# Optimization experiments

Measured on AMD Instinct MI355X. Metric: run time of the kernel, lower is better.

## Reference

```python
import jax, jax.numpy as jnp
import numpy as np

N_NODES = 50000
N_EDGES = 800000
N_GRAPHS = 2000
F = 256          # node feature dim == hidden_dim (required by stacked convs)
HID = 256
L = 4
FP = 1034
BN_EPS = 1e-5


def setup_inputs() -> dict:
    key = jax.random.key(0)
    ks = jax.random.split(key, 20)
    s = 0.05
    x = jax.random.normal(ks[0], (N_NODES, F), dtype=jnp.float32)
    edge_index = jax.random.randint(ks[1], (2, N_EDGES), 0, N_NODES, dtype=jnp.int64)
    edge_attr = jax.random.normal(ks[2], (N_EDGES, 1), dtype=jnp.float32)
    fingerprint = jax.random.uniform(ks[3], (N_GRAPHS, FP), dtype=jnp.float32)
    batch = jnp.sort(jax.random.randint(ks[4], (N_NODES,), 0, N_GRAPHS, dtype=jnp.int64))
    # stacked per-layer conv params: message linear [(F+1)->HID], update linear [HID->HID]
    lin_w = jax.random.normal(ks[5], (L, F + 1, HID), dtype=jnp.float32) * s
    lin_b = jax.random.normal(ks[6], (L, HID), dtype=jnp.float32) * s
    upd_w = jax.random.normal(ks[7], (L, HID, HID), dtype=jnp.float32) * s
    upd_b = jax.random.normal(ks[8], (L, HID), dtype=jnp.float32) * s
    # gated-attention pooling gate_nn: Linear(HID,HID) -> tanh -> Linear(HID,1)
    g1_w = jax.random.normal(ks[9], (HID, HID), dtype=jnp.float32) * s
    g1_b = jax.random.normal(ks[10], (HID,), dtype=jnp.float32) * s
    g2_w = jax.random.normal(ks[11], (HID, 1), dtype=jnp.float32) * s
    g2_b = jax.random.normal(ks[12], (1,), dtype=jnp.float32) * s
    fc1_w = jax.random.normal(ks[13], (HID + FP, HID), dtype=jnp.float32) * s
    fc1_b = jax.random.normal(ks[14], (HID,), dtype=jnp.float32) * s
    bn_gamma = jnp.ones((HID,), dtype=jnp.float32)
    bn_beta = jnp.zeros((HID,), dtype=jnp.float32)
    fc2_w = jax.random.normal(ks[15], (HID, 1), dtype=jnp.float32) * s
    fc2_b = jax.random.normal(ks[16], (1,), dtype=jnp.float32) * s
    return dict(x=x, edge_index=edge_index, edge_attr=edge_attr,
                fingerprint=fingerprint, batch=batch,
                lin_w=lin_w, lin_b=lin_b, upd_w=upd_w, upd_b=upd_b,
                g1_w=g1_w, g1_b=g1_b, g2_w=g2_w, g2_b=g2_b,
                fc1_w=fc1_w, fc1_b=fc1_b, bn_gamma=bn_gamma, bn_beta=bn_beta,
                fc2_w=fc2_w, fc2_b=fc2_b)


def reference(x, edge_index, edge_attr, fingerprint, batch,
              lin_w, lin_b, upd_w, upd_b,
              g1_w, g1_b, g2_w, g2_b,
              fc1_w, fc1_b, bn_gamma, bn_beta, fc2_w, fc2_b):
    n = x.shape[0]
    b = fingerprint.shape[0]
    loop = jnp.arange(n, dtype=edge_index.dtype)
    src = jnp.concatenate([edge_index[0], loop])   # x_j = source nodes (PyG default)
    dst = jnp.concatenate([edge_index[1], loop])   # aggregate at target
    ea = jnp.concatenate([edge_attr, jnp.zeros((n, edge_attr.shape[1]), edge_attr.dtype)], axis=0)
    for l in range(L):
        wn, we = lin_w[l, :F], lin_w[l, F:]        # split concat([x_j, edge_attr]) @ W
        msg = jax.nn.relu(x[src] @ wn + ea @ we + lin_b[l])          # [E+n, HID]
        aggr = jax.ops.segment_sum(msg, dst, num_segments=n)          # scatter-add
        x = jax.nn.relu(aggr @ upd_w[l] + upd_b[l])
    # gated attention pooling
    gate = jax.nn.sigmoid(jnp.tanh(x @ g1_w + g1_b) @ g2_w + g2_b)    # [n, 1]
    pooled = jax.ops.segment_sum(x * gate, batch, num_segments=b)     # [b, HID]
    h = jnp.concatenate([pooled, fingerprint], axis=1) @ fc1_w + fc1_b
    # BatchNorm1d (training mode: biased batch stats)
    mu = jnp.mean(h, axis=0)
    var = jnp.mean((h - mu) ** 2, axis=0)
    h = (h - mu) * jax.lax.rsqrt(var + BN_EPS) * bn_gamma + bn_beta
    h = jax.nn.relu(h)  # dropout is identity in eval mode
    return (h @ fc2_w + fc2_b).squeeze(-1)        # [b]
```

## Files before the change

### kernel.cpp

```cpp
#include <hip/hip_runtime.h>
#include <math.h>

#define HIDF 256
#define FPDIM 1034
#define MPAD 50048

typedef _Float16 f16x8 __attribute__((ext_vector_type(8)));
typedef _Float16 f16x4 __attribute__((ext_vector_type(4)));
typedef float f32x4 __attribute__((ext_vector_type(4)));

__device__ __forceinline__ float relu_f(float v) { return fmaxf(v, 0.f); }

__global__ __launch_bounds__(256) void convxh_k(
    const float* __restrict__ x, _Float16* __restrict__ xh, int n)
{
    int i = blockIdx.x * 256 + threadIdx.x;
    int row = i >> 6;
    if (row >= MPAD) return;
    f16x4 o;
    if (row < n) {
        float4 v = ((const float4*)x)[i];
        o[0] = (_Float16)v.x; o[1] = (_Float16)v.y;
        o[2] = (_Float16)v.z; o[3] = (_Float16)v.w;
    } else {
        o[0] = o[1] = o[2] = o[3] = (_Float16)0.f;
    }
    ((f16x4*)xh)[i] = o;
}

__global__ __launch_bounds__(256) void convw_k(
    const float* __restrict__ w, _Float16* __restrict__ whi,
    _Float16* __restrict__ wlo)
{
    int i = blockIdx.x * 256 + threadIdx.x;
    int nn = i >> 8, kk = i & 255;
    float v = w[kk * 256 + nn];
    _Float16 h = (_Float16)v;
    _Float16 l = (_Float16)(v - (float)h);
    whi[i] = h;
    wlo[i] = l;
}

template <int ACT>
__global__ __launch_bounds__(256) void gemm_f16(
    const _Float16* __restrict__ A, const _Float16* __restrict__ Whi,
    const _Float16* __restrict__ Wlo, const float* __restrict__ bias,
    _Float16* __restrict__ C, int M, int N, int K)
{
    __shared__ _Float16 As[128 * 64];
    __shared__ _Float16 Bh[128 * 64];
    __shared__ _Float16 Bl[128 * 64];
    const int tid = threadIdx.x;
    const int wave = tid >> 6, lane = tid & 63;
    const int m0 = blockIdx.y * 128, n0 = blockIdx.x * 128;
    const int wr = wave >> 1, wc = wave & 1;

    f32x4 acc[4][4];
#pragma unroll
    for (int i = 0; i < 4; ++i)
#pragma unroll
        for (int j = 0; j < 4; ++j) acc[i][j] = (f32x4){0.f, 0.f, 0.f, 0.f};

    const int lrow = lane >> 3;
    const int lcol8 = (lane & 7) * 8;

    for (int k0 = 0; k0 < K; k0 += 64) {
#pragma unroll
        for (int i = 0; i < 4; ++i) {
            int iss = wave * 4 + i;
            int row = 8 * iss + lrow;
            const _Float16* ga = A   + (size_t)(m0 + row) * K + k0 + lcol8;
            const _Float16* gh = Whi + (size_t)(n0 + row) * K + k0 + lcol8;
            const _Float16* gl = Wlo + (size_t)(n0 + row) * K + k0 + lcol8;
            __builtin_amdgcn_global_load_lds(
                (const __attribute__((address_space(1))) void*)ga,
                (__attribute__((address_space(3))) void*)(As + iss * 512), 16, 0, 0);
            __builtin_amdgcn_global_load_lds(
                (const __attribute__((address_space(1))) void*)gh,
                (__attribute__((address_space(3))) void*)(Bh + iss * 512), 16, 0, 0);
            __builtin_amdgcn_global_load_lds(
                (const __attribute__((address_space(1))) void*)gl,
                (__attribute__((address_space(3))) void*)(Bl + iss * 512), 16, 0, 0);
        }
        __syncthreads();
#pragma unroll
        for (int kk = 0; kk < 2; ++kk) {
            const int kb = kk * 32 + (lane >> 4) * 8;
            f16x8 af[4], bh[4], bl[4];
#pragma unroll
            for (int mi = 0; mi < 4; ++mi)
                af[mi] = *(const f16x8*)&As[(wr * 64 + mi * 16 + (lane & 15)) * 64 + kb];
#pragma unroll
            for (int ni = 0; ni < 4; ++ni) {
                int r = (wc * 64 + ni * 16 + (lane & 15)) * 64 + kb;
                bh[ni] = *(const f16x8*)&Bh[r];
                bl[ni] = *(const f16x8*)&Bl[r];
            }
#pragma unroll
            for (int mi = 0; mi < 4; ++mi)
#pragma unroll
                for (int ni = 0; ni < 4; ++ni) {
                    acc[mi][ni] = __builtin_amdgcn_mfma_f32_16x16x32_f16(
                        af[mi], bh[ni], acc[mi][ni], 0, 0, 0);
                    acc[mi][ni] = __builtin_amdgcn_mfma_f32_16x16x32_f16(
                        af[mi], bl[ni], acc[mi][ni], 0, 0, 0);
                }
        }
        __syncthreads();
    }

    const int crow0 = m0 + wr * 64 + (lane >> 4) * 4;
    const int ccol0 = n0 + wc * 64 + (lane & 15);
#pragma unroll
    for (int mi = 0; mi < 4; ++mi) {
#pragma unroll
        for (int ni = 0; ni < 4; ++ni) {
            int col = ccol0 + ni * 16;
            float bv = bias ? bias[col] : 0.f;
#pragma unroll
            for (int r = 0; r < 4; ++r) {
                int row = crow0 + mi * 16 + r;
                float v = acc[mi][ni][r] + bv;
                if (ACT == 1) v = relu_f(v);
                else if (ACT == 2) v = tanhf(v);
                C[(size_t)row * N + col] = (_Float16)v;
            }
        }
    }
}

__global__ void count_k(const int* __restrict__ dst, int* __restrict__ cnt, int E)
{
    int e = blockIdx.x * blockDim.x + threadIdx.x;
    if (e < E) atomicAdd(&cnt[dst[e]], 1);
}

__global__ __launch_bounds__(256) void scan1_k(
    const int* __restrict__ cnt, int* __restrict__ offs,
    int* __restrict__ bsum, int n)
{
    __shared__ int sh[256];
    int t = threadIdx.x, idx = blockIdx.x * 256 + t;
    int v = (idx < n) ? cnt[idx] : 0;
    sh[t] = v;
    __syncthreads();
    for (int o = 1; o < 256; o <<= 1) {
        int a = (t >= o) ? sh[t - o] : 0;
        __syncthreads();
        sh[t] += a;
        __syncthreads();
    }
    if (idx < n) offs[idx] = sh[t] - v;
    if (t == 255) bsum[blockIdx.x] = sh[255];
}

__global__ __launch_bounds__(256) void scan2_k(int* __restrict__ bsum, int nb)
{
    __shared__ int sh[256];
    int t = threadIdx.x;
    int v = (t < nb) ? bsum[t] : 0;
    sh[t] = v;
    __syncthreads();
    for (int o = 1; o < 256; o <<= 1) {
        int a = (t >= o) ? sh[t - o] : 0;
        __syncthreads();
        sh[t] += a;
        __syncthreads();
    }
    if (t < nb) bsum[t] = sh[t] - v;
}

__global__ __launch_bounds__(256) void scan3_k(
    int* __restrict__ offs, const int* __restrict__ bsum,
    int* __restrict__ cursor, int n, int E)
{
    int idx = blockIdx.x * 256 + threadIdx.x;
    if (idx < n) {
        int o = offs[idx] + bsum[blockIdx.x];
        offs[idx] = o;
        cursor[idx] = o;
    }
    if (idx == 0) offs[n] = E;
}

__global__ void scatter_k(const int* __restrict__ dst, const int* __restrict__ src,
                          const float* __restrict__ ea, int* __restrict__ cursor,
                          int* __restrict__ srcS, float* __restrict__ eaS, int E)
{
    int e = blockIdx.x * blockDim.x + threadIdx.x;
    if (e < E) {
        int p = atomicAdd(&cursor[dst[e]], 1);
        srcS[p] = src[e];
        eaS[p] = ea[e];
    }
}

__global__ void start_k(const int* __restrict__ batch, int* __restrict__ start,
                        int n, int B)
{
    int g = blockIdx.x * blockDim.x + threadIdx.x;
    if (g > B) return;
    int lo = 0, hi = n;
    while (lo < hi) {
        int mid = (lo + hi) >> 1;
        if (batch[mid] < g) lo = mid + 1; else hi = mid;
    }
    start[g] = lo;
}

__global__ __launch_bounds__(256) void aggregate_k(
    const _Float16* __restrict__ xw, const float* __restrict__ we,
    const float* __restrict__ lb, const int* __restrict__ srcS,
    const float* __restrict__ eaS, const int* __restrict__ offs,
    _Float16* __restrict__ out, int n)
{
    int w = (blockIdx.x * blockDim.x + threadIdx.x) >> 6;
    if (w >= n) return;
    int lane = threadIdx.x & 63;
    int f = lane << 2;
    float4 we4 = *(const float4*)(we + f);
    float4 lb4 = *(const float4*)(lb + f);
    f16x4 xs = *(const f16x4*)(xw + (size_t)w * HIDF + f);
    float4 acc;
    acc.x = relu_f((float)xs[0] + lb4.x);
    acc.y = relu_f((float)xs[1] + lb4.y);
    acc.z = relu_f((float)xs[2] + lb4.z);
    acc.w = relu_f((float)xs[3] + lb4.w);
    int e0 = offs[w], e1 = offs[w + 1];
    int ii = e0;
    for (; ii + 4 <= e1; ii += 4) {
        int s0 = srcS[ii], s1 = srcS[ii + 1], s2 = srcS[ii + 2], s3 = srcS[ii + 3];
        float a0 = eaS[ii], a1 = eaS[ii + 1], a2 = eaS[ii + 2], a3 = eaS[ii + 3];
        f16x4 v0 = *(const f16x4*)(xw + (size_t)s0 * HIDF + f);
        f16x4 v1 = *(const f16x4*)(xw + (size_t)s1 * HIDF + f);
        f16x4 v2 = *(const f16x4*)(xw + (size_t)s2 * HIDF + f);
        f16x4 v3 = *(const f16x4*)(xw + (size_t)s3 * HIDF + f);
        acc.x += relu_f(fmaf(a0, we4.x, (float)v0[0]) + lb4.x);
        acc.y += relu_f(fmaf(a0, we4.y, (float)v0[1]) + lb4.y);
        acc.z += relu_f(fmaf(a0, we4.z, (float)v0[2]) + lb4.z);
        acc.w += relu_f(fmaf(a0, we4.w, (float)v0[3]) + lb4.w);
        acc.x += relu_f(fmaf(a1, we4.x, (float)v1[0]) + lb4.x);
        acc.y += relu_f(fmaf(a1, we4.y, (float)v1[1]) + lb4.y);
        acc.z += relu_f(fmaf(a1, we4.z, (float)v1[2]) + lb4.z);
        acc.w += relu_f(fmaf(a1, we4.w, (float)v1[3]) + lb4.w);
        acc.x += relu_f(fmaf(a2, we4.x, (float)v2[0]) + lb4.x);
        acc.y += relu_f(fmaf(a2, we4.y, (float)v2[1]) + lb4.y);
        acc.z += relu_f(fmaf(a2, we4.z, (float)v2[2]) + lb4.z);
        acc.w += relu_f(fmaf(a2, we4.w, (float)v2[3]) + lb4.w);
        acc.x += relu_f(fmaf(a3, we4.x, (float)v3[0]) + lb4.x);
        acc.y += relu_f(fmaf(a3, we4.y, (float)v3[1]) + lb4.y);
        acc.z += relu_f(fmaf(a3, we4.z, (float)v3[2]) + lb4.z);
        acc.w += relu_f(fmaf(a3, we4.w, (float)v3[3]) + lb4.w);
    }
    for (; ii < e1; ++ii) {
        int s0 = srcS[ii];
        float a0 = eaS[ii];
        f16x4 v0 = *(const f16x4*)(xw + (size_t)s0 * HIDF + f);
        acc.x += relu_f(fmaf(a0, we4.x, (float)v0[0]) + lb4.x);
        acc.y += relu_f(fmaf(a0, we4.y, (float)v0[1]) + lb4.y);
        acc.z += relu_f(fmaf(a0, we4.z, (float)v0[2]) + lb4.z);
        acc.w += relu_f(fmaf(a0, we4.w, (float)v0[3]) + lb4.w);
    }
    f16x4 o;
    o[0] = (_Float16)acc.x; o[1] = (_Float16)acc.y;
    o[2] = (_Float16)acc.z; o[3] = (_Float16)acc.w;
    *(f16x4*)(out + (size_t)w * HIDF + f) = o;
}

__global__ __launch_bounds__(256) void gate_k(
    const _Float16* __restrict__ t, const float* __restrict__ g2w,
    const float* __restrict__ g2b, float* __restrict__ gate, int n)
{
    int w = (blockIdx.x * blockDim.x + threadIdx.x) >> 6;
    if (w >= n) return;
    int lane = threadIdx.x & 63;
    f16x4 tv = *(const f16x4*)(t + (size_t)w * HIDF + (lane << 2));
    float4 g = *(const float4*)(g2w + (lane << 2));
    float s = (float)tv[0] * g.x + (float)tv[1] * g.y
            + (float)tv[2] * g.z + (float)tv[3] * g.w;
    for (int o = 32; o; o >>= 1) s += __shfl_xor(s, o);
    if (lane == 0) gate[w] = 1.f / (1.f + expf(-(s + g2b[0])));
}

__global__ __launch_bounds__(256) void pool_k(
    const _Float16* __restrict__ x, const float* __restrict__ gate,
    const int* __restrict__ start, float* __restrict__ pooled, int B)
{
    int w = (blockIdx.x * blockDim.x + threadIdx.x) >> 6;
    if (w >= B) return;
    int lane = threadIdx.x & 63;
    int f = lane << 2;
    float4 acc = make_float4(0.f, 0.f, 0.f, 0.f);
    int i0 = start[w], i1 = start[w + 1];
    for (int i = i0; i < i1; ++i) {
        float gi = gate[i];
        f16x4 v = *(const f16x4*)(x + (size_t)i * HIDF + f);
        acc.x = fmaf(gi, (float)v[0], acc.x);
        acc.y = fmaf(gi, (float)v[1], acc.y);
        acc.z = fmaf(gi, (float)v[2], acc.z);
        acc.w = fmaf(gi, (float)v[3], acc.w);
    }
    *(float4*)(pooled + (size_t)w * HIDF + f) = acc;
}

#define FC1_G 8
#define FC1_K (HIDF + FPDIM)
__global__ __launch_bounds__(256) void fc1_k(
    const float* __restrict__ pooled, const float* __restrict__ fp,
    const float* __restrict__ w, const float* __restrict__ b,
    float* __restrict__ h, int B)
{
    __shared__ float in[FC1_G][1292];
    int g0 = blockIdx.x * FC1_G;
    int tid = threadIdx.x;
    for (int r = 0; r < FC1_G; ++r) {
        int g = g0 + r;
        in[r][tid] = (g < B) ? pooled[(size_t)g * HIDF + tid] : 0.f;
        for (int c = tid; c < FPDIM; c += 256)
            in[r][HIDF + c] = (g < B) ? fp[(size_t)g * FPDIM + c] : 0.f;
    }
    __syncthreads();
    int j = tid;
    float acc[FC1_G];
#pragma unroll
    for (int r = 0; r < FC1_G; ++r) acc[r] = b[j];
    int k = 0;
    for (; k + 4 <= FC1_K; k += 4) {
        float w0 = w[(size_t)(k + 0) * HIDF + j];
        float w1 = w[(size_t)(k + 1) * HIDF + j];
        float w2 = w[(size_t)(k + 2) * HIDF + j];
        float w3 = w[(size_t)(k + 3) * HIDF + j];
#pragma unroll
        for (int r = 0; r < FC1_G; ++r) {
            float4 iv = *(const float4*)&in[r][k];
            acc[r] = fmaf(iv.x, w0, acc[r]);
            acc[r] = fmaf(iv.y, w1, acc[r]);
            acc[r] = fmaf(iv.z, w2, acc[r]);
            acc[r] = fmaf(iv.w, w3, acc[r]);
        }
    }
    for (; k < FC1_K; ++k) {
        float wk = w[(size_t)k * HIDF + j];
#pragma unroll
        for (int r = 0; r < FC1_G; ++r) acc[r] = fmaf(in[r][k], wk, acc[r]);
    }
    for (int r = 0; r < FC1_G; ++r) {
        int g = g0 + r;
        if (g < B) h[(size_t)g * HIDF + j] = acc[r];
    }
}

__global__ __launch_bounds__(256) void bnstats_k(
    const float* __restrict__ h, float* __restrict__ mu,
    float* __restrict__ rs, int B)
{
    int j = blockIdx.x;
    int tid = threadIdx.x;
    float s = 0.f, s2 = 0.f;
    for (int g = tid; g < B; g += 256) {
        float v = h[(size_t)g * HIDF + j];
        s += v;
        s2 = fmaf(v, v, s2);
    }
    __shared__ float sh[256], sh2[256];
    sh[tid] = s; sh2[tid] = s2;
    __syncthreads();
    for (int o = 128; o; o >>= 1) {
        if (tid < o) { sh[tid] += sh[tid + o]; sh2[tid] += sh2[tid + o]; }
        __syncthreads();
    }
    if (tid == 0) {
        float m = sh[0] / (float)B;
        float var = sh2[0] / (float)B - m * m;
        if (var < 0.f) var = 0.f;
        mu[j] = m;
        rs[j] = rsqrtf(var + 1e-5f);
    }
}

__global__ __launch_bounds__(256) void final_k(
    const float* __restrict__ h, const float* __restrict__ mu,
    const float* __restrict__ rs, const float* __restrict__ gamma,
    const float* __restrict__ beta, const float* __restrict__ w2,
    const float* __restrict__ b2, float* __restrict__ out, int B)
{
    int g = blockIdx.x;
    int j = threadIdx.x;
    float v = h[(size_t)g * HIDF + j];
    v = (v - mu[j]) * rs[j] * gamma[j] + beta[j];
    v = relu_f(v);
    float term = v * w2[j];
    __shared__ float sh[256];
    sh[j] = term;
    __syncthreads();
    for (int o = 128; o; o >>= 1) {
        if (j < o) sh[j] += sh[j + o];
        __syncthreads();
    }
    if (j == 0) out[g] = sh[0] + b2[0];
}

extern "C" void kernel_launch(void* const* d_in, const int* in_sizes, int n_in,
                              void* d_out, int out_size, void* d_ws, size_t ws_size,
                              hipStream_t stream)
{
    const float* x      = (const float*)d_in[0];
    const int*   ei     = (const int*)d_in[1];
    const float* ea     = (const float*)d_in[2];
    const float* fp     = (const float*)d_in[3];
    const int*   batch  = (const int*)d_in[4];
    const float* lin_w  = (const float*)d_in[5];
    const float* lin_b  = (const float*)d_in[6];
    const float* upd_w  = (const float*)d_in[7];
    const float* upd_b  = (const float*)d_in[8];
    const float* g1w    = (const float*)d_in[9];
    const float* g1b    = (const float*)d_in[10];
    const float* g2w    = (const float*)d_in[11];
    const float* g2b    = (const float*)d_in[12];
    const float* fc1w   = (const float*)d_in[13];
    const float* fc1b   = (const float*)d_in[14];
    const float* gamma  = (const float*)d_in[15];
    const float* beta   = (const float*)d_in[16];
    const float* fc2w   = (const float*)d_in[17];
    const float* fc2b   = (const float*)d_in[18];
    float* out = (float*)d_out;

    const int n = in_sizes[0] / HIDF;
    const int E = in_sizes[1] / 2;
    const int B = in_sizes[3] / FPDIM;
    const int L = in_sizes[5] / (257 * 256);
    const int* srcArr = ei;
    const int* dstArr = ei + E;
    const int nb = (n + 255) / 256;

    char* w = (char*)d_ws;
    _Float16* xh   = (_Float16*)w;  w += (size_t)MPAD * HIDF * 2;
    _Float16* bufA = (_Float16*)w;  w += (size_t)MPAD * HIDF * 2;
    _Float16* bufB = (_Float16*)w;  w += (size_t)MPAD * HIDF * 2;
    _Float16* whi = (_Float16*)w;  w += (size_t)9 * 65536 * 2;
    _Float16* wlo = (_Float16*)w;  w += (size_t)9 * 65536 * 2;
    int*   srcS   = (int*)w;    w += (size_t)E * 4;
    float* eaS    = (float*)w;  w += (size_t)E * 4;
    int*   offs   = (int*)w;    w += ((size_t)n + 4) * 4;
    int*   cursor = (int*)w;    w += ((size_t)n + 4) * 4;
    int*   cnt    = (int*)w;    w += (size_t)n * 4;
    int*   bsum   = (int*)w;    w += 256 * 4;
    int*   startA = (int*)w;    w += ((size_t)B + 4) * 4;
    float* gateA  = (float*)w;  w += (size_t)n * 4;
    float* pooled = (float*)w;  w += (size_t)B * HIDF * 4;
    float* h      = (float*)w;  w += (size_t)B * HIDF * 4;
    float* mu     = (float*)w;  w += 256 * 4;
    float* rs     = (float*)w;  w += 256 * 4;

    hipMemsetAsync(cnt, 0, (size_t)n * 4, stream);
    count_k<<<(E + 255) / 256, 256, 0, stream>>>(dstArr, cnt, E);
    scan1_k<<<nb, 256, 0, stream>>>(cnt, offs, bsum, n);
    scan2_k<<<1, 256, 0, stream>>>(bsum, nb);
    scan3_k<<<nb, 256, 0, stream>>>(offs, bsum, cursor, n, E);
    scatter_k<<<(E + 255) / 256, 256, 0, stream>>>(dstArr, srcArr, ea, cursor, srcS, eaS, E);
    start_k<<<(B + 256) / 256, 256, 0, stream>>>(batch, startA, n, B);

    convxh_k<<<(MPAD * 64 + 255) / 256, 256, 0, stream>>>(x, xh, n);
    for (int l = 0; l < L; ++l) {
        convw_k<<<256, 256, 0, stream>>>(lin_w + (size_t)l * 257 * 256,
                                         whi + (size_t)l * 65536, wlo + (size_t)l * 65536);
        convw_k<<<256, 256, 0, stream>>>(upd_w + (size_t)l * 65536,
                                         whi + (size_t)(4 + l) * 65536, wlo + (size_t)(4 + l) * 65536);
    }
    convw_k<<<256, 256, 0, stream>>>(g1w, whi + (size_t)8 * 65536, wlo + (size_t)8 * 65536);

    dim3 ggm(HIDF / 128, MPAD / 128);
    for (int l = 0; l < L; ++l) {
        const float* we = lin_w + (size_t)l * 257 * 256 + 256 * 256;
        const float* lb = lin_b + (size_t)l * 256;
        gemm_f16<0><<<ggm, 256, 0, stream>>>(xh, whi + (size_t)l * 65536,
                                             wlo + (size_t)l * 65536, nullptr,
                                             bufA, MPAD, HIDF, HIDF);
        aggregate_k<<<(n * 64 + 255) / 256, 256, 0, stream>>>(
            bufA, we, lb, srcS, eaS, offs, bufB, n);
        gemm_f16<1><<<ggm, 256, 0, stream>>>(bufB, whi + (size_t)(4 + l) * 65536,
                                             wlo + (size_t)(4 + l) * 65536,
                                             upd_b + (size_t)l * 256, xh, MPAD, HIDF, HIDF);
    }

    gemm_f16<2><<<ggm, 256, 0, stream>>>(xh, whi + (size_t)8 * 65536,
                                         wlo + (size_t)8 * 65536, g1b,
                                         bufA, MPAD, HIDF, HIDF);
    gate_k<<<(n * 64 + 255) / 256, 256, 0, stream>>>(bufA, g2w, g2b, gateA, n);
    pool_k<<<(B * 64 + 255) / 256, 256, 0, stream>>>(xh, gateA, startA, pooled, B);

    fc1_k<<<(B + FC1_G - 1) / FC1_G, 256, 0, stream>>>(pooled, fp, fc1w, fc1b, h, B);
    bnstats_k<<<256, 256, 0, stream>>>(h, mu, rs, B);
    final_k<<<B, 256, 0, stream>>>(h, mu, rs, gamma, beta, fc2w, fc2b, out, B);
}
```

Before: 730.9 us.

## Move fc1 to split-fp16 MFMA GEMM, fold message bias into GEMM, deepen aggregate unroll

The scalar fp32 fc1 kernel is replaced by conversion kernels that pad and split the concatenated input and the weights into fp16 hi/lo pairs, followed by a three-term MFMA GEMM. The message bias is added in the first GEMM's epilogue rather than per edge inside aggregation. The aggregation loop is also unrolled to eight edges so more gathers are in flight at once. The fc1 path adds conversion passes and extra workspace, and the bias is now added before rounding to fp16 instead of after, which can shift results slightly.

After: 717.5 us. Within noise of the previous version (-1.8%).

```diff
diff --git a/kernel.cpp b/kernel.cpp
--- a/kernel.cpp
+++ b/kernel.cpp
@@ -4,6 +4,8 @@
 #define HIDF 256
 #define FPDIM 1034
 #define MPAD 50048
+#define FCM 2048
+#define FCK 1344
 
 typedef _Float16 f16x8 __attribute__((ext_vector_type(8)));
 typedef _Float16 f16x4 __attribute__((ext_vector_type(4)));
@@ -41,6 +43,38 @@
     wlo[i] = l;
 }
 
+__global__ __launch_bounds__(256) void convfc1a_k(
+    const float* __restrict__ pooled, const float* __restrict__ fp,
+    _Float16* __restrict__ ahi, _Float16* __restrict__ alo, int B)
+{
+    int i = blockIdx.x * 256 + threadIdx.x;
+    if (i >= FCM * FCK) return;
+    int row = i / FCK, col = i - row * FCK;
+    float v = 0.f;
+    if (row < B) {
+        if (col < HIDF) v = pooled[(size_t)row * HIDF + col];
+        else if (col < HIDF + FPDIM) v = fp[(size_t)row * FPDIM + (col - HIDF)];
+    }
+    _Float16 h = (_Float16)v;
+    _Float16 l = (_Float16)(v - (float)h);
+    ahi[i] = h;
+    alo[i] = l;
+}
+
+__global__ __launch_bounds__(256) void convfc1w_k(
+    const float* __restrict__ w, _Float16* __restrict__ whi,
+    _Float16* __restrict__ wlo)
+{
+    int i = blockIdx.x * 256 + threadIdx.x;
+    if (i >= HIDF * FCK) return;
+    int nn = i / FCK, kk = i - nn * FCK;
+    float v = (kk < HIDF + FPDIM) ? w[(size_t)kk * HIDF + nn] : 0.f;
+    _Float16 h = (_Float16)v;
+    _Float16 l = (_Float16)(v - (float)h);
+    whi[i] = h;
+    wlo[i] = l;
+}
+
 template <int ACT>
 __global__ __launch_bounds__(256) void gemm_f16(
     const _Float16* __restrict__ A, const _Float16* __restrict__ Whi,
@@ -129,6 +163,102 @@
     }
 }
 
+__global__ __launch_bounds__(256) void gemm_fc1(
+    const _Float16* __restrict__ Ahi, const _Float16* __restrict__ Alo,
+    const _Float16* __restrict__ Whi, const _Float16* __restrict__ Wlo,
+    const float* __restrict__ bias, float* __restrict__ C,
+    int Mv, int N, int K)
+{
+    __shared__ _Float16 Ah[128 * 64];
+    __shared__ _Float16 Al[128 * 64];
+    __shared__ _Float16 Bh[128 * 64];
+    __shared__ _Float16 Bl[128 * 64];
+    const int tid = threadIdx.x;
+    const int wave = tid >> 6, lane = tid & 63;
+    const int m0 = blockIdx.y * 128, n0 = blockIdx.x * 128;
+    const int wr = wave >> 1, wc = wave & 1;
+
+    f32x4 acc[4][4];
+#pragma unroll
+    for (int i = 0; i < 4; ++i)
+#pragma unroll
+        for (int j = 0; j < 4; ++j) acc[i][j] = (f32x4){0.f, 0.f, 0.f, 0.f};
+
+    const int lrow = lane >> 3;
+    const int lcol8 = (lane & 7) * 8;
+
+    for (int k0 = 0; k0 < K; k0 += 64) {
+#pragma unroll
+        for (int i = 0; i < 4; ++i) {
+            int iss = wave * 4 + i;
+            int row = 8 * iss + lrow;
+            const _Float16* gah = Ahi + (size_t)(m0 + row) * K + k0 + lcol8;
+            const _Float16* gal = Alo + (size_t)(m0 + row) * K + k0 + lcol8;
+            const _Float16* gbh = Whi + (size_t)(n0 + row) * K + k0 + lcol8;
+            const _Float16* gbl = Wlo + (size_t)(n0 + row) * K + k0 + lcol8;
+            __builtin_amdgcn_global_load_lds(
+                (const __attribute__((address_space(1))) void*)gah,
+                (__attribute__((address_space(3))) void*)(Ah + iss * 512), 16, 0, 0);
+            __builtin_amdgcn_global_load_lds(
+                (const __attribute__((address_space(1))) void*)gal,
+                (__attribute__((address_space(3))) void*)(Al + iss * 512), 16, 0, 0);
+            __builtin_amdgcn_global_load_lds(
+                (const __attribute__((address_space(1))) void*)gbh,
+                (__attribute__((address_space(3))) void*)(Bh + iss * 512), 16, 0, 0);
+            __builtin_amdgcn_global_load_lds(
+                (const __attribute__((address_space(1))) void*)gbl,
+                (__attribute__((address_space(3))) void*)(Bl + iss * 512), 16, 0, 0);
+        }
+        __syncthreads();
+#pragma unroll
+        for (int kk = 0; kk < 2; ++kk) {
+            const int kb = kk * 32 + (lane >> 4) * 8;
+            f16x8 ah[4], al[4], bh[4], bl[4];
+#pragma unroll
+            for (int mi = 0; mi < 4; ++mi) {
+                int r = (wr * 64 + mi * 16 + (lane & 15)) * 64 + kb;
+                ah[mi] = *(const f16x8*)&Ah[r];
+                al[mi] = *(const f16x8*)&Al[r];
+            }
+#pragma unroll
+            for (int ni = 0; ni < 4; ++ni) {
+                int r = (wc * 64 + ni * 16 + (lane & 15)) * 64 + kb;
+                bh[ni] = *(const f16x8*)&Bh[r];
+                bl[ni] = *(const f16x8*)&Bl[r];
+            }
+#pragma unroll
+            for (int mi = 0; mi < 4; ++mi)
+#pragma unroll
+                for (int ni = 0; ni < 4; ++ni) {
+                    acc[mi][ni] = __builtin_amdgcn_mfma_f32_16x16x32_f16(
+                        ah[mi], bh[ni], acc[mi][ni], 0, 0, 0);
+                    acc[mi][ni] = __builtin_amdgcn_mfma_f32_16x16x32_f16(
+                        ah[mi], bl[ni], acc[mi][ni], 0, 0, 0);
+                    acc[mi][ni] = __builtin_amdgcn_mfma_f32_16x16x32_f16(
+                        al[mi], bh[ni], acc[mi][ni], 0, 0, 0);
+                }
+        }
+        __syncthreads();
+    }
+
+    const int crow0 = m0 + wr * 64 + (lane >> 4) * 4;
+    const int ccol0 = n0 + wc * 64 + (lane & 15);
+#pragma unroll
+    for (int mi = 0; mi < 4; ++mi) {
+#pragma unroll
+        for (int ni = 0; ni < 4; ++ni) {
+            int col = ccol0 + ni * 16;
+            float bv = bias[col];
+#pragma unroll
+            for (int r = 0; r < 4; ++r) {
+                int row = crow0 + mi * 16 + r;
+                if (row < Mv)
+                    C[(size_t)row * N + col] = acc[mi][ni][r] + bv;
+            }
+        }
+    }
+}
+
 __global__ void count_k(const int* __restrict__ dst, int* __restrict__ cnt, int E)
 {
     int e = blockIdx.x * blockDim.x + threadIdx.x;
@@ -210,56 +340,61 @@
 
 __global__ __launch_bounds__(256) void aggregate_k(
     const _Float16* __restrict__ xw, const float* __restrict__ we,
-    const float* __restrict__ lb, const int* __restrict__ srcS,
-    const float* __restrict__ eaS, const int* __restrict__ offs,
-    _Float16* __restrict__ out, int n)
+    const int* __restrict__ srcS, const float* __restrict__ eaS,
+    const int* __restrict__ offs, _Float16* __restrict__ out, int n)
 {
     int w = (blockIdx.x * blockDim.x + threadIdx.x) >> 6;
     if (w >= n) return;
     int lane = threadIdx.x & 63;
     int f = lane << 2;
     float4 we4 = *(const float4*)(we + f);
-    float4 lb4 = *(const float4*)(lb + f);
     f16x4 xs = *(const f16x4*)(xw + (size_t)w * HIDF + f);
     float4 acc;
-    acc.x = relu_f((float)xs[0] + lb4.x);
-    acc.y = relu_f((float)xs[1] + lb4.y);
-    acc.z = relu_f((float)xs[2] + lb4.z);
-    acc.w = relu_f((float)xs[3] + lb4.w);
+    acc.x = relu_f((float)xs[0]);
+    acc.y = relu_f((float)xs[1]);
+    acc.z = relu_f((float)xs[2]);
+    acc.w = relu_f((float)xs[3]);
     int e0 = offs[w], e1 = offs[w + 1];
     int ii = e0;
-    for (; ii + 4 <= e1; ii += 4) {
-        int s0 = srcS[ii], s1 = srcS[ii + 1], s2 = srcS[ii + 2], s3 = srcS[ii + 3];
-        float a0 = eaS[ii], a1 = eaS[ii + 1], a2 = eaS[ii + 2], a3 = eaS[ii + 3];
-        f16x4 v0 = *(const f16x4*)(xw + (size_t)s0 * HIDF + f);
-        f16x4 v1 = *(const f16x4*)(xw + (size_t)s1 * HIDF + f);
-        f16x4 v2 = *(const f16x4*)(xw + (size_t)s2 * HIDF + f);
-        f16x4 v3 = *(const f16x4*)(xw + (size_t)s3 * HIDF + f);
-        acc.x += relu_f(fmaf(a0, we4.x, (float)v0[0]) + lb4.x);
-        acc.y += relu_f(fmaf(a0, we4.y, (float)v0[1]) + lb4.y);
-        acc.z += relu_f(fmaf(a0, we4.z, (float)v0[2]) + lb4.z);
-        acc.w += relu_f(fmaf(a0, we4.w, (float)v0[3]) + lb4.w);
-        acc.x += relu_f(fmaf(a1, we4.x, (float)v1[0]) + lb4.x);
-        acc.y += relu_f(fmaf(a1, we4.y, (float)v1[1]) + lb4.y);
-        acc.z += relu_f(fmaf(a1, we4.z, (float)v1[2]) + lb4.z);
-        acc.w += relu_f(fmaf(a1, we4.w, (float)v1[3]) + lb4.w);
-        acc.x += relu_f(fmaf(a2, we4.x, (float)v2[0]) + lb4.x);
-        acc.y += relu_f(fmaf(a2, we4.y, (float)v2[1]) + lb4.y);
-        acc.z += relu_f(fmaf(a2, we4.z, (float)v2[2]) + lb4.z);
-        acc.w += relu_f(fmaf(a2, we4.w, (float)v2[3]) + lb4.w);
-        acc.x += relu_f(fmaf(a3, we4.x, (float)v3[0]) + lb4.x);
-        acc.y += relu_f(fmaf(a3, we4.y, (float)v3[1]) + lb4.y);
-        acc.z += relu_f(fmaf(a3, we4.z, (float)v3[2]) + lb4.z);
-        acc.w += relu_f(fmaf(a3, we4.w, (float)v3[3]) + lb4.w);
+    for (; ii + 8 <= e1; ii += 8) {
+        int s[8]; float a[8]; f16x4 v[8];
+#pragma unroll
+        for (int j = 0; j < 8; ++j) { s[j] = srcS[ii + j]; a[j] = eaS[ii + j]; }
+#pragma unroll
+        for (int j = 0; j < 8; ++j)
+            v[j] = *(const f16x4*)(xw + (size_t)s[j] * HIDF + f);
+#pragma unroll
+        for (int j = 0; j < 8; ++j) {
+            acc.x += relu_f(fmaf(a[j], we4.x, (float)v[j][0]));
+            acc.y += relu_f(fmaf(a[j], we4.y, (float)v[j][1]));
+            acc.z += relu_f(fmaf(a[j], we4.z, (float)v[j][2]));
+            acc.w += relu_f(fmaf(a[j], we4.w, (float)v[j][3]));
+        }
+    }
+    if (ii + 4 <= e1) {
+        int s[4]; float a[4]; f16x4 v[4];
+#pragma unroll
+        for (int j = 0; j < 4; ++j) { s[j] = srcS[ii + j]; a[j] = eaS[ii + j]; }
+#pragma unroll
+        for (int j = 0; j < 4; ++j)
+            v[j] = *(const f16x4*)(xw + (size_t)s[j] * HIDF + f);
+#pragma unroll
+        for (int j = 0; j < 4; ++j) {
+            acc.x += relu_f(fmaf(a[j], we4.x, (float)v[j][0]));
+            acc.y += relu_f(fmaf(a[j], we4.y, (float)v[j][1]));
+            acc.z += relu_f(fmaf(a[j], we4.z, (float)v[j][2]));
+            acc.w += relu_f(fmaf(a[j], we4.w, (float)v[j][3]));
+        }
+        ii += 4;
     }
     for (; ii < e1; ++ii) {
         int s0 = srcS[ii];
         float a0 = eaS[ii];
         f16x4 v0 = *(const f16x4*)(xw + (size_t)s0 * HIDF + f);
-        acc.x += relu_f(fmaf(a0, we4.x, (float)v0[0]) + lb4.x);
-        acc.y += relu_f(fmaf(a0, we4.y, (float)v0[1]) + lb4.y);
-        acc.z += relu_f(fmaf(a0, we4.z, (float)v0[2]) + lb4.z);
-        acc.w += relu_f(fmaf(a0, we4.w, (float)v0[3]) + lb4.w);
+        acc.x += relu_f(fmaf(a0, we4.x, (float)v0[0]));
+        acc.y += relu_f(fmaf(a0, we4.y, (float)v0[1]));
+        acc.z += relu_f(fmaf(a0, we4.z, (float)v0[2]));
+        acc.w += relu_f(fmaf(a0, we4.w, (float)v0[3]));
     }
     f16x4 o;
     o[0] = (_Float16)acc.x; o[1] = (_Float16)acc.y;
@@ -301,53 +436,6 @@
         acc.w = fmaf(gi, (float)v[3], acc.w);
     }
     *(float4*)(pooled + (size_t)w * HIDF + f) = acc;
-}
-
-#define FC1_G 8
-#define FC1_K (HIDF + FPDIM)
-__global__ __launch_bounds__(256) void fc1_k(
-    const float* __restrict__ pooled, const float* __restrict__ fp,
-    const float* __restrict__ w, const float* __restrict__ b,
-    float* __restrict__ h, int B)
-{
-    __shared__ float in[FC1_G][1292];
-    int g0 = blockIdx.x * FC1_G;
-    int tid = threadIdx.x;
-    for (int r = 0; r < FC1_G; ++r) {
-        int g = g0 + r;
-        in[r][tid] = (g < B) ? pooled[(size_t)g * HIDF + tid] : 0.f;
-        for (int c = tid; c < FPDIM; c += 256)
-            in[r][HIDF + c] = (g < B) ? fp[(size_t)g * FPDIM + c] : 0.f;
-    }
-    __syncthreads();
-    int j = tid;
-    float acc[FC1_G];
-#pragma unroll
-    for (int r = 0; r < FC1_G; ++r) acc[r] = b[j];
-    int k = 0;
-    for (; k + 4 <= FC1_K; k += 4) {
-        float w0 = w[(size_t)(k + 0) * HIDF + j];
-        float w1 = w[(size_t)(k + 1) * HIDF + j];
-        float w2 = w[(size_t)(k + 2) * HIDF + j];
-        float w3 = w[(size_t)(k + 3) * HIDF + j];
-#pragma unroll
-        for (int r = 0; r < FC1_G; ++r) {
-            float4 iv = *(const float4*)&in[r][k];
-            acc[r] = fmaf(iv.x, w0, acc[r]);
-            acc[r] = fmaf(iv.y, w1, acc[r]);
-            acc[r] = fmaf(iv.z, w2, acc[r]);
-            acc[r] = fmaf(iv.w, w3, acc[r]);
-        }
-    }
-    for (; k < FC1_K; ++k) {
-        float wk = w[(size_t)k * HIDF + j];
-#pragma unroll
-        for (int r = 0; r < FC1_G; ++r) acc[r] = fmaf(in[r][k], wk, acc[r]);
-    }
-    for (int r = 0; r < FC1_G; ++r) {
-        int g = g0 + r;
-        if (g < B) h[(size_t)g * HIDF + j] = acc[r];
-    }
 }
 
 __global__ __launch_bounds__(256) void bnstats_k(
@@ -439,6 +527,10 @@
     _Float16* bufB = (_Float16*)w;  w += (size_t)MPAD * HIDF * 2;
     _Float16* whi = (_Float16*)w;  w += (size_t)9 * 65536 * 2;
     _Float16* wlo = (_Float16*)w;  w += (size_t)9 * 65536 * 2;
+    _Float16* fahi = (_Float16*)w; w += (size_t)FCM * FCK * 2;
+    _Float16* falo = (_Float16*)w; w += (size_t)FCM * FCK * 2;
+    _Float16* fwhi = (_Float16*)w; w += (size_t)HIDF * FCK * 2;
+    _Float16* fwlo = (_Float16*)w; w += (size_t)HIDF * FCK * 2;
     int*   srcS   = (int*)w;    w += (size_t)E * 4;
     float* eaS    = (float*)w;  w += (size_t)E * 4;
     int*   offs   = (int*)w;    w += ((size_t)n + 4) * 4;
@@ -468,16 +560,17 @@
                                          whi + (size_t)(4 + l) * 65536, wlo + (size_t)(4 + l) * 65536);
     }
     convw_k<<<256, 256, 0, stream>>>(g1w, whi + (size_t)8 * 65536, wlo + (size_t)8 * 65536);
+    convfc1w_k<<<(HIDF * FCK + 255) / 256, 256, 0, stream>>>(fc1w, fwhi, fwlo);
 
     dim3 ggm(HIDF / 128, MPAD / 128);
     for (int l = 0; l < L; ++l) {
         const float* we = lin_w + (size_t)l * 257 * 256 + 256 * 256;
         const float* lb = lin_b + (size_t)l * 256;
         gemm_f16<0><<<ggm, 256, 0, stream>>>(xh, whi + (size_t)l * 65536,
-                                             wlo + (size_t)l * 65536, nullptr,
+                                             wlo + (size_t)l * 65536, lb,
                                              bufA, MPAD, HIDF, HIDF);
         aggregate_k<<<(n * 64 + 255) / 256, 256, 0, stream>>>(
-            bufA, we, lb, srcS, eaS, offs, bufB, n);
+            bufA, we, srcS, eaS, offs, bufB, n);
         gemm_f16<1><<<ggm, 256, 0, stream>>>(bufB, whi + (size_t)(4 + l) * 65536,
                                              wlo + (size_t)(4 + l) * 65536,
                                              upd_b + (size_t)l * 256, xh, MPAD, HIDF, HIDF);
@@ -489,7 +582,9 @@
     gate_k<<<(n * 64 + 255) / 256, 256, 0, stream>>>(bufA, g2w, g2b, gateA, n);
     pool_k<<<(B * 64 + 255) / 256, 256, 0, stream>>>(xh, gateA, startA, pooled, B);
 
-    fc1_k<<<(B + FC1_G - 1) / FC1_G, 256, 0, stream>>>(pooled, fp, fc1w, fc1b, h, B);
+    convfc1a_k<<<(FCM * FCK + 255) / 256, 256, 0, stream>>>(pooled, fp, fahi, falo, B);
+    dim3 ggf(HIDF / 128, FCM / 128);
+    gemm_fc1<<<ggf, 256, 0, stream>>>(fahi, falo, fwhi, fwlo, fc1b, h, B, HIDF, FCK);
     bnstats_k<<<256, 256, 0, stream>>>(h, mu, rs, B);
     final_k<<<B, 256, 0, stream>>>(h, mu, rs, gamma, beta, fc2w, fc2b, out, B);
 }
```
